# Optimization experiments

Hardware: AMD Instinct MI355X
Metric: run time of the kernel (lower is better)

Reference implementation:

```python
import jax, jax.numpy as jnp
import numpy as np

N_NODES = 50000
N_EDGES = 800000
H = 8            # n_heads
VAL_CH = 64      # h * n value channels
D = 3            # SO(3) degree dimension (2l+1, l=1)
T = 16           # key dim per head


def setup_inputs() -> dict:
    key = jax.random.key(0)
    k1, k2, k3, k4 = jax.random.split(key, 4)
    v = jax.random.normal(k1, (N_EDGES, VAL_CH, D), dtype=jnp.float32)
    k = jax.random.normal(k2, (N_EDGES, H, T), dtype=jnp.float32)
    q = jax.random.normal(k3, (N_NODES, H, T), dtype=jnp.float32)
    dst = jax.random.randint(k4, (N_EDGES,), 0, N_NODES, dtype=jnp.int32)
    return {"v": v, "k": k, "q": q, "dst": dst}


def reference(v, k, q, dst):
    # v: [E, h*n, d] edge values; k: [E, h, t] edge keys; q: [N, h, t] node queries
    E = v.shape[0]
    N = q.shape[0]
    h = k.shape[1]
    t = k.shape[2]
    vh = v.reshape(E, h, -1, v.shape[-1])          # [E, h, n, d]
    scale = 1.0 / np.sqrt(h * t).astype(np.float32)  # sqrt(f_key.deg_size)
    # per-edge attention logits: dot(k_e, q_dst(e)) per head
    logits = jnp.einsum('eht,eht->eh', k, q[dst]) * scale   # [E, h]
    # edge softmax over incoming edges of each destination node
    m = jax.ops.segment_max(logits, dst, num_segments=N)    # [N, h]
    m = jax.lax.stop_gradient(m)
    ex = jnp.exp(logits - m[dst])                           # [E, h]
    denom = jax.ops.segment_sum(ex, dst, num_segments=N)    # [N, h]
    a = ex / denom[dst]                                     # [E, h]
    # weighted message + scatter-sum to destination nodes
    msg = a[:, :, None, None] * vh                          # [E, h, n, d]
    out = jax.ops.segment_sum(msg, dst, num_segments=N)     # [N, h, n, d]
    return out.reshape(N, -1, v.shape[-1])                  # [N, h*n, d]
```

## Files before the change

### kernel.cpp

```cpp
#include <hip/hip_runtime.h>

#define HH 8
#define CAPL 128
#define BSTRIDE 256

static constexpr float SCALE = 0.08838834764831843f;

struct f3 {
  float x, y, z;
};

typedef float vf4 __attribute__((ext_vector_type(4)));

__global__ __launch_bounds__(256) void edge_kernel(
    const float* __restrict__ k, const float* __restrict__ q,
    const int* __restrict__ dst, int* __restrict__ cursor,
    int* __restrict__ eid, float* __restrict__ lgS, int E) {
  int t = blockIdx.x * 256 + threadIdx.x;
  int e = t >> 3;
  if (e >= E) return;
  int h = t & 7;
  int lane = threadIdx.x & 63;
  int d = dst[e];

  const vf4* kk = (const vf4*)(k + (size_t)e * 128 + h * 16);
  const vf4* qq = (const vf4*)(q + (size_t)d * 128 + h * 16);
  vf4 a0 = __builtin_nontemporal_load(kk + 0);
  vf4 a1 = __builtin_nontemporal_load(kk + 1);
  vf4 a2 = __builtin_nontemporal_load(kk + 2);
  vf4 a3 = __builtin_nontemporal_load(kk + 3);
  vf4 b0 = qq[0], b1 = qq[1], b2 = qq[2], b3 = qq[3];
  float acc = a0.x * b0.x + a0.y * b0.y + a0.z * b0.z + a0.w * b0.w;
  acc += a1.x * b1.x + a1.y * b1.y + a1.z * b1.z + a1.w * b1.w;
  acc += a2.x * b2.x + a2.y * b2.y + a2.z * b2.z + a2.w * b2.w;
  acc += a3.x * b3.x + a3.y * b3.y + a3.z * b3.z + a3.w * b3.w;
  float lg = acc * SCALE;

  int pos = 0;
  if (h == 0) pos = atomicAdd(&cursor[d], 1);
  pos = __shfl(pos, lane & ~7, 64);
  if (pos < BSTRIDE) {
    size_t slot = (size_t)d * BSTRIDE + pos;
    if (h == 0) eid[slot] = e;
    lgS[slot * HH + h] = lg;
  }
}

__global__ __launch_bounds__(256) void node_kernel(
    const float* __restrict__ v, const float* __restrict__ lgS,
    const int* __restrict__ cursor, const int* __restrict__ eid,
    float* __restrict__ out, int N) {
  __shared__ int eidL[4][CAPL];
  __shared__ float wL[4][CAPL * HH];

  int tid = threadIdx.x;
  int wave = tid >> 6;
  int lane = tid & 63;
  int node = blockIdx.x * 4 + wave;
  if (node >= N) return;

  int deg = min(cursor[node], BSTRIDE);
  int nl = min(deg, CAPL);
  const int* bucket = eid + (size_t)node * BSTRIDE;
  const float* lgN = lgS + (size_t)node * (BSTRIDE * HH);
  const char* vB = (const char*)v;
  uint32_t vlane = (uint32_t)(lane * 12);

  for (int i = lane; i < nl; i += 64) eidL[wave][i] = bucket[i];

  float m = -1e30f;
  for (int i = lane; i < nl * 8; i += 64) {
    float lg = lgN[i];
    wL[wave][i] = lg;
    m = fmaxf(m, lg);
  }
  for (int i = CAPL * 8 + lane; i < deg * 8; i += 64)
    m = fmaxf(m, lgN[i]);
  m = fmaxf(m, __shfl_xor(m, 8, 64));
  m = fmaxf(m, __shfl_xor(m, 16, 64));
  m = fmaxf(m, __shfl_xor(m, 32, 64));

  float s = 0.f;
  for (int i = lane; i < nl * 8; i += 64) {
    float ex = __expf(wL[wave][i] - m);
    wL[wave][i] = ex;
    s += ex;
  }
  for (int i = CAPL * 8 + lane; i < deg * 8; i += 64)
    s += __expf(lgN[i] - m);
  s += __shfl_xor(s, 8, 64);
  s += __shfl_xor(s, 16, 64);
  s += __shfl_xor(s, 32, 64);
  float inv = (s > 0.f) ? 1.0f / s : 0.f;

  int hc = lane >> 3;
  float minv = __shfl(inv, hc, 64);
  float m_c = __shfl(m, hc, 64);
  float a0 = 0.f, a1 = 0.f, a2 = 0.f;
  int i = 0;
  for (; i + 4 <= nl; i += 4) {
    int e0 = eidL[wave][i + 0];
    int e1 = eidL[wave][i + 1];
    int e2 = eidL[wave][i + 2];
    int e3 = eidL[wave][i + 3];
    float w0 = wL[wave][(i + 0) * 8 + hc];
    float w1 = wL[wave][(i + 1) * 8 + hc];
    float w2 = wL[wave][(i + 2) * 8 + hc];
    float w3 = wL[wave][(i + 3) * 8 + hc];
    f3 v0 = *(const f3*)(vB + (uint32_t)e0 * 768u + vlane);
    f3 v1 = *(const f3*)(vB + (uint32_t)e1 * 768u + vlane);
    f3 v2 = *(const f3*)(vB + (uint32_t)e2 * 768u + vlane);
    f3 v3 = *(const f3*)(vB + (uint32_t)e3 * 768u + vlane);
    a0 += w0 * v0.x + w1 * v1.x + w2 * v2.x + w3 * v3.x;
    a1 += w0 * v0.y + w1 * v1.y + w2 * v2.y + w3 * v3.y;
    a2 += w0 * v0.z + w1 * v1.z + w2 * v2.z + w3 * v3.z;
  }
  for (; i < nl; ++i) {
    int e = eidL[wave][i];
    float w = wL[wave][i * 8 + hc];
    f3 vv = *(const f3*)(vB + (uint32_t)e * 768u + vlane);
    a0 += w * vv.x;
    a1 += w * vv.y;
    a2 += w * vv.z;
  }
  for (; i < deg; ++i) {
    int e = bucket[i];
    float w = __expf(lgN[i * 8 + hc] - m_c);
    f3 vv = *(const f3*)(vB + (uint32_t)e * 768u + vlane);
    a0 += w * vv.x;
    a1 += w * vv.y;
    a2 += w * vv.z;
  }
  a0 *= minv;
  a1 *= minv;
  a2 *= minv;

  f3* op = (f3*)((char*)out + (uint32_t)node * 768u + vlane);
  op->x = a0;
  op->y = a1;
  op->z = a2;
}

extern "C" void kernel_launch(void* const* d_in, const int* in_sizes, int n_in,
                              void* d_out, int out_size, void* d_ws,
                              size_t ws_size, hipStream_t stream) {
  const float* v = (const float*)d_in[0];
  const float* k = (const float*)d_in[1];
  const float* q = (const float*)d_in[2];
  const int* dst = (const int*)d_in[3];
  float* out = (float*)d_out;

  const int E = in_sizes[3];
  const int N = in_sizes[2] / (HH * 16);

  char* ws = (char*)d_ws;
  size_t off = 0;
  auto take = [&](size_t bytes) {
    void* p = ws + off;
    off += (bytes + 255) & ~(size_t)255;
    return p;
  };
  int* cursor = (int*)take((size_t)N * sizeof(int));
  int* eid = (int*)take((size_t)N * BSTRIDE * sizeof(int));
  float* lgS = (float*)take((size_t)N * BSTRIDE * HH * sizeof(float));

  hipMemsetAsync(cursor, 0, (size_t)N * sizeof(int), stream);
  edge_kernel<<<(E * 8 + 255) / 256, 256, 0, stream>>>(k, q, dst, cursor, eid,
                                                       lgS, E);
  node_kernel<<<(N + 3) / 4, 256, 0, stream>>>(v, lgS, cursor, eid, out, N);
}
```

Baseline: 318.9 us.

## Split node gather into per-node softmax and per-edge atomic scatter

Replaces the node-centric gather of v rows with three phases: edge logits stored in edge order, a per-node softmax that normalizes those logits in place through the bucket indices, and a per-edge kernel that streams v contiguously and atomically adds weighted values into a zeroed output. The aim is to trade random 768-byte gathers of v for coalesced streaming reads. In exchange it adds about 150M float atomics to global memory, a memset of the output, and an extra kernel launch, and the summation order becomes nondeterministic. Edges beyond the 256-slot bucket cap would still be scattered but left unnormalized.

Result: slower. 687.8 us (+115.6%).

```diff
diff --git a/kernel.cpp b/kernel.cpp
--- a/kernel.cpp
+++ b/kernel.cpp
@@ -1,26 +1,20 @@
 #include <hip/hip_runtime.h>
 
 #define HH 8
-#define CAPL 128
 #define BSTRIDE 256
 
 static constexpr float SCALE = 0.08838834764831843f;
 
-struct f3 {
-  float x, y, z;
-};
-
 typedef float vf4 __attribute__((ext_vector_type(4)));
 
-__global__ __launch_bounds__(256) void edge_kernel(
+__global__ __launch_bounds__(256) void edge_logits_kernel(
     const float* __restrict__ k, const float* __restrict__ q,
     const int* __restrict__ dst, int* __restrict__ cursor,
-    int* __restrict__ eid, float* __restrict__ lgS, int E) {
+    int* __restrict__ eid, float* __restrict__ lgE, int E) {
   int t = blockIdx.x * 256 + threadIdx.x;
   int e = t >> 3;
   if (e >= E) return;
   int h = t & 7;
-  int lane = threadIdx.x & 63;
   int d = dst[e];
 
   const vf4* kk = (const vf4*)(k + (size_t)e * 128 + h * 16);
@@ -34,111 +28,74 @@
   acc += a1.x * b1.x + a1.y * b1.y + a1.z * b1.z + a1.w * b1.w;
   acc += a2.x * b2.x + a2.y * b2.y + a2.z * b2.z + a2.w * b2.w;
   acc += a3.x * b3.x + a3.y * b3.y + a3.z * b3.z + a3.w * b3.w;
-  float lg = acc * SCALE;
+  lgE[t] = acc * SCALE;
 
-  int pos = 0;
-  if (h == 0) pos = atomicAdd(&cursor[d], 1);
-  pos = __shfl(pos, lane & ~7, 64);
-  if (pos < BSTRIDE) {
-    size_t slot = (size_t)d * BSTRIDE + pos;
-    if (h == 0) eid[slot] = e;
-    lgS[slot * HH + h] = lg;
+  if (h == 0) {
+    int pos = atomicAdd(&cursor[d], 1);
+    if (pos < BSTRIDE) eid[d * BSTRIDE + pos] = e;
   }
 }
 
-__global__ __launch_bounds__(256) void node_kernel(
-    const float* __restrict__ v, const float* __restrict__ lgS,
-    const int* __restrict__ cursor, const int* __restrict__ eid,
-    float* __restrict__ out, int N) {
-  __shared__ int eidL[4][CAPL];
-  __shared__ float wL[4][CAPL * HH];
-
-  int tid = threadIdx.x;
-  int wave = tid >> 6;
-  int lane = tid & 63;
+__global__ __launch_bounds__(256) void softmax_kernel(
+    float* __restrict__ lgE, const int* __restrict__ cursor,
+    const int* __restrict__ eid, int N) {
+  __shared__ int eidL[4][BSTRIDE];
+  int wave = threadIdx.x >> 6;
+  int lane = threadIdx.x & 63;
   int node = blockIdx.x * 4 + wave;
   if (node >= N) return;
 
   int deg = min(cursor[node], BSTRIDE);
-  int nl = min(deg, CAPL);
-  const int* bucket = eid + (size_t)node * BSTRIDE;
-  const float* lgN = lgS + (size_t)node * (BSTRIDE * HH);
-  const char* vB = (const char*)v;
-  uint32_t vlane = (uint32_t)(lane * 12);
+  const int* bucket = eid + node * BSTRIDE;
+  for (int i = lane; i < deg; i += 64) eidL[wave][i] = bucket[i];
 
-  for (int i = lane; i < nl; i += 64) eidL[wave][i] = bucket[i];
+  int n8 = deg * 8;
 
   float m = -1e30f;
-  for (int i = lane; i < nl * 8; i += 64) {
-    float lg = lgN[i];
-    wL[wave][i] = lg;
-    m = fmaxf(m, lg);
+  for (int i = lane; i < n8; i += 64) {
+    int e = eidL[wave][i >> 3];
+    m = fmaxf(m, lgE[e * 8 + (i & 7)]);
   }
-  for (int i = CAPL * 8 + lane; i < deg * 8; i += 64)
-    m = fmaxf(m, lgN[i]);
   m = fmaxf(m, __shfl_xor(m, 8, 64));
   m = fmaxf(m, __shfl_xor(m, 16, 64));
   m = fmaxf(m, __shfl_xor(m, 32, 64));
 
   float s = 0.f;
-  for (int i = lane; i < nl * 8; i += 64) {
-    float ex = __expf(wL[wave][i] - m);
-    wL[wave][i] = ex;
-    s += ex;
+  for (int i = lane; i < n8; i += 64) {
+    int e = eidL[wave][i >> 3];
+    s += __expf(lgE[e * 8 + (i & 7)] - m);
   }
-  for (int i = CAPL * 8 + lane; i < deg * 8; i += 64)
-    s += __expf(lgN[i] - m);
   s += __shfl_xor(s, 8, 64);
   s += __shfl_xor(s, 16, 64);
   s += __shfl_xor(s, 32, 64);
   float inv = (s > 0.f) ? 1.0f / s : 0.f;
 
-  int hc = lane >> 3;
-  float minv = __shfl(inv, hc, 64);
-  float m_c = __shfl(m, hc, 64);
-  float a0 = 0.f, a1 = 0.f, a2 = 0.f;
-  int i = 0;
-  for (; i + 4 <= nl; i += 4) {
-    int e0 = eidL[wave][i + 0];
-    int e1 = eidL[wave][i + 1];
-    int e2 = eidL[wave][i + 2];
-    int e3 = eidL[wave][i + 3];
-    float w0 = wL[wave][(i + 0) * 8 + hc];
-    float w1 = wL[wave][(i + 1) * 8 + hc];
-    float w2 = wL[wave][(i + 2) * 8 + hc];
-    float w3 = wL[wave][(i + 3) * 8 + hc];
-    f3 v0 = *(const f3*)(vB + (uint32_t)e0 * 768u + vlane);
-    f3 v1 = *(const f3*)(vB + (uint32_t)e1 * 768u + vlane);
-    f3 v2 = *(const f3*)(vB + (uint32_t)e2 * 768u + vlane);
-    f3 v3 = *(const f3*)(vB + (uint32_t)e3 * 768u + vlane);
-    a0 += w0 * v0.x + w1 * v1.x + w2 * v2.x + w3 * v3.x;
-    a1 += w0 * v0.y + w1 * v1.y + w2 * v2.y + w3 * v3.y;
-    a2 += w0 * v0.z + w1 * v1.z + w2 * v2.z + w3 * v3.z;
+  for (int i = lane; i < n8; i += 64) {
+    int e = eidL[wave][i >> 3];
+    float lg = lgE[e * 8 + (i & 7)];
+    lgE[e * 8 + (i & 7)] = __expf(lg - m) * inv;
   }
-  for (; i < nl; ++i) {
-    int e = eidL[wave][i];
-    float w = wL[wave][i * 8 + hc];
-    f3 vv = *(const f3*)(vB + (uint32_t)e * 768u + vlane);
-    a0 += w * vv.x;
-    a1 += w * vv.y;
-    a2 += w * vv.z;
+}
+
+__global__ __launch_bounds__(256) void scatter_kernel(
+    const float* __restrict__ v, const float* __restrict__ lgE,
+    const int* __restrict__ dst, float* __restrict__ out, int E) {
+  int w = blockIdx.x * 4 + (threadIdx.x >> 6);
+  if (w >= E) return;
+  int lane = threadIdx.x & 63;
+  int e = w;
+  int d = dst[e];
+
+  const float* vr = v + (size_t)e * 192;
+  const float* wr = lgE + (size_t)e * 8;
+  float* orow = out + (size_t)d * 192;
+#pragma unroll
+  for (int i = 0; i < 3; ++i) {
+    int idx = i * 64 + lane;
+    float wt = wr[idx / 24];
+    float val = __builtin_nontemporal_load(vr + idx);
+    atomicAdd(orow + idx, wt * val);
   }
-  for (; i < deg; ++i) {
-    int e = bucket[i];
-    float w = __expf(lgN[i * 8 + hc] - m_c);
-    f3 vv = *(const f3*)(vB + (uint32_t)e * 768u + vlane);
-    a0 += w * vv.x;
-    a1 += w * vv.y;
-    a2 += w * vv.z;
-  }
-  a0 *= minv;
-  a1 *= minv;
-  a2 *= minv;
-
-  f3* op = (f3*)((char*)out + (uint32_t)node * 768u + vlane);
-  op->x = a0;
-  op->y = a1;
-  op->z = a2;
 }
 
 extern "C" void kernel_launch(void* const* d_in, const int* in_sizes, int n_in,
@@ -162,10 +119,13 @@
   };
   int* cursor = (int*)take((size_t)N * sizeof(int));
   int* eid = (int*)take((size_t)N * BSTRIDE * sizeof(int));
-  float* lgS = (float*)take((size_t)N * BSTRIDE * HH * sizeof(float));
+  float* lgE = (float*)take((size_t)E * HH * sizeof(float));
 
   hipMemsetAsync(cursor, 0, (size_t)N * sizeof(int), stream);
-  edge_kernel<<<(E * 8 + 255) / 256, 256, 0, stream>>>(k, q, dst, cursor, eid,
-                                                       lgS, E);
-  node_kernel<<<(N + 3) / 4, 256, 0, stream>>>(v, lgS, cursor, eid, out, N);
+  hipMemsetAsync(out, 0, (size_t)out_size * sizeof(float), stream);
+
+  edge_logits_kernel<<<(E * 8 + 255) / 256, 256, 0, stream>>>(k, q, dst, cursor,
+                                                              eid, lgE, E);
+  softmax_kernel<<<(N + 3) / 4, 256, 0, stream>>>(lgE, cursor, eid, N);
+  scatter_kernel<<<(E + 3) / 4, 256, 0, stream>>>(v, lgE, dst, out, E);
 }
```
